# Kernel tuning notes

Hardware: AMD Instinct MI355X
Metric: run time of the kernel (lower is better)

Reference implementation:

```python
import jax, jax.numpy as jnp
import numpy as np

N_EMBD = 1024
N_HEAD = 16
HEAD_DIM = N_EMBD // N_HEAD
LN_EPS = 1e-5


def setup_inputs() -> dict:
    key = jax.random.key(0)
    ks = jax.random.split(key, 8)
    B, T, C = 4, 2048, N_EMBD
    s = lambda fan_in: 1.0 / np.sqrt(fan_in)
    return {
        'x': jax.random.normal(ks[0], (B, T, C), dtype=jnp.float32),
        'w_qkv': jax.random.normal(ks[1], (C, 3 * C), dtype=jnp.float32) * s(C),
        'b_qkv': jnp.zeros((3 * C,), dtype=jnp.float32),
        'ln1_g': jnp.ones((C,), dtype=jnp.float32),
        'ln1_b': jnp.zeros((C,), dtype=jnp.float32),
        'w_fc1': jax.random.normal(ks[2], (C, 4 * C), dtype=jnp.float32) * s(C),
        'b_fc1': jnp.zeros((4 * C,), dtype=jnp.float32),
        'w_fc2': jax.random.normal(ks[3], (4 * C, C), dtype=jnp.float32) * s(4 * C),
        'b_fc2': jnp.zeros((C,), dtype=jnp.float32),
        'ln2_g': jnp.ones((C,), dtype=jnp.float32),
        'ln2_b': jnp.zeros((C,), dtype=jnp.float32),
    }


def _layernorm(x, g, b):
    mu = jnp.mean(x, axis=-1, keepdims=True)
    var = jnp.mean(jnp.square(x - mu), axis=-1, keepdims=True)
    return (x - mu) * jax.lax.rsqrt(var + LN_EPS) * g + b


def _attention(x, w_qkv, b_qkv):
    B, T, C = x.shape
    qkv = x @ w_qkv + b_qkv                      # [B,T,3C]
    q, k, v = jnp.split(qkv, 3, axis=-1)
    q = q.reshape(B, T, N_HEAD, HEAD_DIM)
    k = k.reshape(B, T, N_HEAD, HEAD_DIM)
    v = v.reshape(B, T, N_HEAD, HEAD_DIM)
    scores = jnp.einsum('bqhd,bkhd->bhqk', q, k) / np.sqrt(HEAD_DIM).astype(np.float32)
    causal = jnp.tril(jnp.ones((T, T), dtype=bool))
    scores = jnp.where(causal, scores, -jnp.inf)
    attn = jax.nn.softmax(scores, axis=-1)       # [B,H,T,T]
    y = jnp.einsum('bhqk,bkhd->bqhd', attn, v)
    return y.reshape(B, T, C)


def reference(x, w_qkv, b_qkv, ln1_g, ln1_b, w_fc1, b_fc1, w_fc2, b_fc2, ln2_g, ln2_b):
    # Block: x = ln1(x + attn(x)); x = ln2(x + mlp(x))   (post-LN residual)
    x = _layernorm(x + _attention(x, w_qkv, b_qkv), ln1_g, ln1_b)
    h = jax.nn.gelu(x @ w_fc1 + b_fc1, approximate=False)
    mlp = h @ w_fc2 + b_fc2
    x = _layernorm(x + mlp, ln2_g, ln2_b)
    return x
```

## Files before the change

kernel.cpp:

```cpp
#include <hip/hip_runtime.h>
#include <cstdint>
#include <cstddef>

#define TB 4
#define TT 2048
#define TC 1024
#define NH 16
#define HD 64
#define MROWS (TB * TT)

typedef __bf16 bf16;
typedef unsigned short u16;
typedef __bf16 bf16x8 __attribute__((ext_vector_type(8)));
typedef float floatx4 __attribute__((ext_vector_type(4)));
typedef unsigned short ushort8 __attribute__((ext_vector_type(8)));
typedef unsigned short ushort4v __attribute__((ext_vector_type(4)));

#define LOG2E 1.4426950408889634f

static __device__ __forceinline__ u16 f2bfbits(float f) {
    bf16 b = (bf16)f;
    return __builtin_bit_cast(u16, b);
}

#if __has_builtin(__builtin_amdgcn_exp2f)
#define EXP2F(x) __builtin_amdgcn_exp2f(x)
#else
#define EXP2F(x) exp2f(x)
#endif

static __device__ __forceinline__ void gld_lds16(const u16* g, const u16* lds) {
    __builtin_amdgcn_global_load_lds(
        (const __attribute__((address_space(1))) unsigned int*)(uintptr_t)g,
        (__attribute__((address_space(3))) unsigned int*)(unsigned int)(uintptr_t)lds,
        16, 0, 0);
}

__global__ __launch_bounds__(256) void prep_kernel(
    const float* __restrict__ x, u16* __restrict__ xb,
    const float* __restrict__ w_qkv, u16* __restrict__ wqkvT,
    const float* __restrict__ w_fc1, u16* __restrict__ wfc1T,
    const float* __restrict__ w_fc2, u16* __restrict__ wfc2T)
{
    const int tid = threadIdx.x;
    int blk = blockIdx.x;
    if (blk < 8192) {
        const int i = blk * 256 + tid;
        float4 v = reinterpret_cast<const float4*>(x)[i];
        ushort4v o;
        o.x = f2bfbits(v.x); o.y = f2bfbits(v.y); o.z = f2bfbits(v.z); o.w = f2bfbits(v.w);
        reinterpret_cast<ushort4v*>(xb)[i] = o;
        return;
    }
    blk -= 8192;
    const float* in; u16* out; int K, N, bx, by;
    if (blk < 3072)      { in = w_qkv; out = wqkvT; K = TC;     N = 3 * TC; bx = blk % 96;  by = blk / 96; }
    else if (blk < 7168) { blk -= 3072; in = w_fc1; out = wfc1T; K = TC;    N = 4 * TC; bx = blk & 127; by = blk >> 7; }
    else                 { blk -= 7168; in = w_fc2; out = wfc2T; K = 4 * TC; N = TC;    bx = blk & 31;  by = blk >> 5; }
    __shared__ float tile[32][33];
    const int n0 = bx * 32, k0 = by * 32;
    const int tx = tid & 31, ty = tid >> 5;
    for (int r = 0; r < 32; r += 8)
        tile[ty + r][tx] = in[(size_t)(k0 + ty + r) * N + n0 + tx];
    __syncthreads();
    for (int r = 0; r < 32; r += 8)
        out[(size_t)(n0 + ty + r) * K + k0 + tx] = f2bfbits(tile[tx][ty + r]);
}

template <int GELU>
__global__ __launch_bounds__(512, 2) void gemm256_kernel(
    const u16* __restrict__ A, const u16* __restrict__ Bt,
    const float* __restrict__ bias, u16* __restrict__ Cmat,
    int Nb, int Mt, int Ksz)
{
    __shared__ u16 As[4 * 8192];
    __shared__ u16 Bs[4 * 8192];
    const int tid  = threadIdx.x;
    const int wave = tid >> 6, lane = tid & 63;
    const int quad = lane >> 4, l16 = lane & 15;
    const int wm = (wave >> 2) * 128, wn = (wave & 3) * 64;
    const int Nsz = Nb * 256;
    const int bid = blockIdx.x;
    const int xcd = bid & 7, qb = bid >> 3;
    const int m0 = (xcd * (Mt >> 3) + qb / Nb) * 256;
    const int n0 = (qb % Nb) * 256;

    const int srow = tid >> 2;
    const int sc8  = ((tid & 3) ^ ((tid >> 3) & 3)) * 8;
    const u16* aP = A  + (size_t)(m0 + srow) * Ksz + sc8;
    const u16* bP = Bt + (size_t)(n0 + srow) * Ksz + sc8;
    const size_t half2 = (size_t)128 * Ksz;
    const int sdst = wave * 512;

    const int slot = quad ^ ((l16 >> 1) & 3);
    const int aRd = (wm + l16) * 32 + slot * 8;
    const int bRd = (wn + l16) * 32 + slot * 8;

    floatx4 acc[8][4];
#pragma unroll
    for (int i = 0; i < 8; i++)
#pragma unroll
        for (int j = 0; j < 4; j++)
            acc[i][j] = (floatx4){0.f, 0.f, 0.f, 0.f};

    const int nt = Ksz >> 6;

#define SA(g, kh) do { const u16* s_ = aP + (g) * 64 + (kh) * 32; \
    u16* d_ = As + (((g) & 1) * 2 + (kh)) * 8192 + sdst; \
    gld_lds16(s_, d_); gld_lds16(s_ + half2, d_ + 4096); } while (0)
#define SB(g, kh) do { const u16* s_ = bP + (g) * 64 + (kh) * 32; \
    u16* d_ = Bs + (((g) & 1) * 2 + (kh)) * 8192 + sdst; \
    gld_lds16(s_, d_); gld_lds16(s_ + half2, d_ + 4096); } while (0)

    SA(0, 0); SB(0, 0); SA(0, 1); SB(0, 1); SA(1, 0); SB(1, 0);
    asm volatile("s_waitcnt vmcnt(4)" ::: "memory");
    __builtin_amdgcn_sched_barrier(0);
    __builtin_amdgcn_s_barrier();

#define PHASE(CH, KH, STAGE_STMT, TAILWAIT) do { \
    const u16* ab_ = As + (p * 2 + (KH)) * 8192 + aRd + (CH) * 2048; \
    const u16* bb_ = Bs + (p * 2 + (KH)) * 8192 + bRd; \
    bf16x8 af_[4], bf_[4]; \
    _Pragma("unroll") \
    for (int i_ = 0; i_ < 4; i_++) \
        af_[i_] = *reinterpret_cast<const bf16x8*>(ab_ + i_ * 512); \
    _Pragma("unroll") \
    for (int j_ = 0; j_ < 4; j_++) \
        bf_[j_] = *reinterpret_cast<const bf16x8*>(bb_ + j_ * 512); \
    STAGE_STMT; \
    __builtin_amdgcn_s_barrier(); \
    asm volatile("s_waitcnt lgkmcnt(0)" ::: "memory"); \
    __builtin_amdgcn_sched_barrier(0); \
    __builtin_amdgcn_s_setprio(1); \
    _Pragma("unroll") \
    for (int i_ = 0; i_ < 4; i_++) \
    _Pragma("unroll") \
    for (int j_ = 0; j_ < 4; j_++) \
        acc[(CH) * 4 + i_][j_] = __builtin_amdgcn_mfma_f32_16x16x32_bf16( \
            af_[i_], bf_[j_], acc[(CH) * 4 + i_][j_], 0, 0, 0); \
    __builtin_amdgcn_s_setprio(0); \
    TAILWAIT; \
    __builtin_amdgcn_s_barrier(); \
} while (0)

    for (int g = 0; g < nt; ++g) {
        const int p = g & 1;
        PHASE(0, 0, if (g + 1 < nt) SA(g + 1, 1), );
        PHASE(1, 0, if (g + 1 < nt) SB(g + 1, 1), );
        PHASE(1, 1, if (g + 2 < nt) SA(g + 2, 0), );
        PHASE(0, 1, if (g + 2 < nt) SB(g + 2, 0),
              if (g < nt - 2) { asm volatile("s_waitcnt vmcnt(4)" ::: "memory"); }
              else           { asm volatile("s_waitcnt vmcnt(0)" ::: "memory"); }
              __builtin_amdgcn_sched_barrier(0));
    }
#undef PHASE
#undef SA
#undef SB

    float bv[4];
#pragma unroll
    for (int j = 0; j < 4; j++) bv[j] = bias[n0 + wn + j * 16 + l16];
    const int odd = l16 & 1;
#pragma unroll
    for (int i = 0; i < 8; i++) {
        const int row0 = m0 + wm + i * 16 + quad * 4;
#pragma unroll
        for (int j = 0; j < 4; j++) {
            float v[4];
#pragma unroll
            for (int r = 0; r < 4; r++) {
                float t = acc[i][j][r] + bv[j];
                if (GELU) {
                    float u = t * (0.7978845608f + 0.0356774081f * t * t);
                    float e = EXP2F(u * (2.0f * LOG2E));
                    t = t - t * __builtin_amdgcn_rcpf(e + 1.0f);
                }
                v[r] = t;
            }
            float pv0 = __shfl_xor(v[0], 1), pv1 = __shfl_xor(v[1], 1);
            float pv2 = __shfl_xor(v[2], 1), pv3 = __shfl_xor(v[3], 1);
            float lo0 = odd ? pv2 : v[0];
            float hi0 = odd ? v[2] : pv0;
            float lo1 = odd ? pv3 : v[1];
            float hi1 = odd ? v[3] : pv1;
            unsigned int d0 = (unsigned int)f2bfbits(lo0) | ((unsigned int)f2bfbits(hi0) << 16);
            unsigned int d1 = (unsigned int)f2bfbits(lo1) | ((unsigned int)f2bfbits(hi1) << 16);
            const int row  = row0 + odd * 2;
            const int colp = n0 + wn + j * 16 + (l16 & ~1);
            *reinterpret_cast<unsigned int*>(Cmat + (size_t)row * Nsz + colp)       = d0;
            *reinterpret_cast<unsigned int*>(Cmat + (size_t)(row + 1) * Nsz + colp) = d1;
        }
    }
}

template <int GELU>
__global__ __launch_bounds__(256, 2) void gemm_bt128_kernel(
    const u16* __restrict__ A, const u16* __restrict__ Bt,
    const float* __restrict__ bias, u16* __restrict__ Cmat,
    int Nb, int Ksz)
{
    __shared__ u16 As[128 * 64];
    __shared__ u16 Bs[128 * 64];
    const int tid  = threadIdx.x;
    const int wave = tid >> 6, lane = tid & 63;
    const int quad = lane >> 4, l16 = lane & 15;
    const int Nsz = Nb * 128;
    const int bid = blockIdx.x;
    const int xcd = bid & 7, qb = bid >> 3;
    const int m0 = (xcd * 8 + qb / Nb) * 128;
    const int n0 = (qb % Nb) * 128;
    const int wm = (wave >> 1) * 64, wn = (wave & 1) * 64;

    const int srow = lane >> 3;
    const int scol = ((lane & 7) ^ srow) * 8;
    const u16* ap = A  + (size_t)(m0 + wave * 32 + srow) * Ksz + scol;
    const u16* bp = Bt + (size_t)(n0 + wave * 32 + srow) * Ksz + scol;
    const size_t astep = (size_t)8 * Ksz;

    floatx4 acc[4][4];
#pragma unroll
    for (int i = 0; i < 4; i++)
#pragma unroll
        for (int j = 0; j < 4; j++)
            acc[i][j] = (floatx4){0.f, 0.f, 0.f, 0.f};

    const int l7 = l16 & 7;

    for (int k0 = 0; k0 < Ksz; k0 += 64) {
        __syncthreads();
#pragma unroll
        for (int d = 0; d < 4; d++)
            gld_lds16(ap + d * astep, As + (wave * 4 + d) * 512);
#pragma unroll
        for (int d = 0; d < 4; d++)
            gld_lds16(bp + d * astep, Bs + (wave * 4 + d) * 512);
        ap += 64; bp += 64;
        __syncthreads();

#pragma unroll
        for (int t = 0; t < 2; t++) {
            const int po = ((t * 4 + quad) ^ l7) * 8;
            bf16x8 af[4], bfr[4];
#pragma unroll
            for (int i = 0; i < 4; i++)
                af[i] = *reinterpret_cast<const bf16x8*>(As + (wm + i * 16 + l16) * 64 + po);
#pragma unroll
            for (int j = 0; j < 4; j++)
                bfr[j] = *reinterpret_cast<const bf16x8*>(Bs + (wn + j * 16 + l16) * 64 + po);
#pragma unroll
            for (int i = 0; i < 4; i++)
#pragma unroll
                for (int j = 0; j < 4; j++)
                    acc[i][j] = __builtin_amdgcn_mfma_f32_16x16x32_bf16(af[i], bfr[j], acc[i][j], 0, 0, 0);
        }
    }

    float bv[4];
#pragma unroll
    for (int j = 0; j < 4; j++) bv[j] = bias[n0 + wn + j * 16 + l16];
    const int odd = l16 & 1;
#pragma unroll
    for (int i = 0; i < 4; i++) {
        const int row0 = m0 + wm + i * 16 + quad * 4;
#pragma unroll
        for (int j = 0; j < 4; j++) {
            float v[4];
#pragma unroll
            for (int r = 0; r < 4; r++) {
                float t = acc[i][j][r] + bv[j];
                if (GELU) {
                    float u = t * (0.7978845608f + 0.0356774081f * t * t);
                    float e = EXP2F(u * (2.0f * LOG2E));
                    t = t - t * __builtin_amdgcn_rcpf(e + 1.0f);
                }
                v[r] = t;
            }
            float pv0 = __shfl_xor(v[0], 1), pv1 = __shfl_xor(v[1], 1);
            float pv2 = __shfl_xor(v[2], 1), pv3 = __shfl_xor(v[3], 1);
            float lo0 = odd ? pv2 : v[0];
            float hi0 = odd ? v[2] : pv0;
            float lo1 = odd ? pv3 : v[1];
            float hi1 = odd ? v[3] : pv1;
            unsigned int d0 = (unsigned int)f2bfbits(lo0) | ((unsigned int)f2bfbits(hi0) << 16);
            unsigned int d1 = (unsigned int)f2bfbits(lo1) | ((unsigned int)f2bfbits(hi1) << 16);
            const int row  = row0 + odd * 2;
            const int colp = n0 + wn + j * 16 + (l16 & ~1);
            *reinterpret_cast<unsigned int*>(Cmat + (size_t)row * Nsz + colp)       = d0;
            *reinterpret_cast<unsigned int*>(Cmat + (size_t)(row + 1) * Nsz + colp) = d1;
        }
    }
}

__global__ __launch_bounds__(512) void attn_kernel(const u16* __restrict__ qkv,
                                                   u16* __restrict__ y)
{
    __shared__ u16 Ks[2 * 64 * 64];
    __shared__ u16 Vt[2 * 64 * 64];
    __shared__ u16 Pw[8][16 * 64];
    const int tid  = threadIdx.x;
    const int wave = tid >> 6, lane = tid & 63;
    const int quad = lane >> 4, l16 = lane & 15;
    const int l7   = l16 & 7;
    const int h = blockIdx.y, b = blockIdx.z;
    const int rowbase = b * TT;
    const int S3C = 3 * TC;

    const int srow = (tid >> 3) & 31;
    const int c8   = (tid & 7) * 8;
    const int pcK  = ((tid & 7) ^ (srow & 7)) * 8;
    const int pvb  = (srow + ((tid & 7) << 2)) & 31;
    const bool kRole = (tid < 256);
    const int pcr = (quad ^ l7) * 8;
    unsigned int* const vtw = (unsigned int*)Vt;

    for (int pass = 0; pass < 2; pass++) {
        const int qt   = pass ? (15 - (int)blockIdx.x) : (int)blockIdx.x;
        const int q0b  = qt * 128;
        const int q0w  = q0b + wave * 16;
        const int kend = q0b + 128;

        __syncthreads();

        bf16x8 qf0, qf1;
        {
            const u16* qrow = qkv + (size_t)(rowbase + q0w + l16) * S3C + h * HD + quad * 8;
            bf16x8 t0 = *reinterpret_cast<const bf16x8*>(qrow);
            bf16x8 t1 = *reinterpret_cast<const bf16x8*>(qrow + 32);
#pragma unroll
            for (int i = 0; i < 8; i++) {
                t0[i] = (bf16)((float)t0[i] * (0.125f * LOG2E));
                t1[i] = (bf16)((float)t1[i] * (0.125f * LOG2E));
            }
            qf0 = t0; qf1 = t1;
        }

        float m_s = -__builtin_inff(), l_s = 0.f;
        floatx4 o_acc[4];
#pragma unroll
        for (int n = 0; n < 4; n++) o_acc[n] = (floatx4){0.f, 0.f, 0.f, 0.f};

        const u16* gp = kRole
            ? qkv + (size_t)(rowbase + srow) * S3C + TC + h * HD + c8
            : qkv + (size_t)(rowbase + 2 * srow) * S3C + 2 * TC + h * HD + c8;
        const size_t g2 = kRole ? (size_t)32 * S3C : (size_t)S3C;
        ushort8 r0 = *reinterpret_cast<const ushort8*>(gp);
        ushort8 r1 = *reinterpret_cast<const ushort8*>(gp + g2);

        int buf = 0;
        for (int k0 = 0; k0 < kend; k0 += 64) {
            if (kRole) {
                u16* kb = Ks + buf * 4096;
                *reinterpret_cast<ushort8*>(kb + srow * 64 + pcK)        = r0;
                *reinterpret_cast<ushort8*>(kb + (srow + 32) * 64 + pcK) = r1;
            } else {
                unsigned int* vb = vtw + buf * 2048;
#pragma unroll
                for (int j = 0; j < 8; j++) {
                    unsigned int pk = (unsigned int)r0[j] | ((unsigned int)r1[j] << 16);
                    vb[(c8 + j) * 32 + (pvb ^ (j << 2))] = pk;
                }
            }
            __syncthreads();

            if (k0 + 64 < kend) {
                const u16* gn = gp + (size_t)(k0 + 64) * S3C;
                r0 = *reinterpret_cast<const ushort8*>(gn);
                r1 = *reinterpret_cast<const ushort8*>(gn + g2);
            }

            if (k0 <= q0w + 15) {
                const u16* ksb = Ks + buf * 4096;
                floatx4 st[4];
#pragma unroll
                for (int t = 0; t < 4; t++) {
                    const u16* krowp = ksb + (t * 16 + l16) * 64;
                    bf16x8 ka  = *reinterpret_cast<const bf16x8*>(krowp + pcr);
                    bf16x8 kb2 = *reinterpret_cast<const bf16x8*>(krowp + (pcr ^ 32));
                    floatx4 s = (floatx4){0.f, 0.f, 0.f, 0.f};
                    s = __builtin_amdgcn_mfma_f32_16x16x32_bf16(ka, qf0, s, 0, 0, 0);
                    s = __builtin_amdgcn_mfma_f32_16x16x32_bf16(kb2, qf1, s, 0, 0, 0);
                    st[t] = s;
                }
                float v[16];
                if (k0 + 63 > q0w) {
                    const int kq = k0 - q0w;
#pragma unroll
                    for (int t = 0; t < 4; t++)
#pragma unroll
                        for (int r = 0; r < 4; r++)
                            v[t * 4 + r] = (t * 16 + quad * 4 + r + kq > l16)
                                               ? -__builtin_inff() : st[t][r];
                } else {
#pragma unroll
                    for (int t = 0; t < 4; t++)
#pragma unroll
                        for (int r = 0; r < 4; r++)
                            v[t * 4 + r] = st[t][r];
                }
                float mx = v[0];
#pragma unroll
                for (int i = 1; i < 16; i++) mx = fmaxf(mx, v[i]);
                mx = fmaxf(mx, __shfl_xor(mx, 16));
                mx = fmaxf(mx, __shfl_xor(mx, 32));
                const float mnew  = fmaxf(m_s, mx);
                const float alpha = EXP2F(m_s - mnew);
                float rs = 0.f;
                u16* const pwb = Pw[wave] + l16 * 64;
#pragma unroll
                for (int t = 0; t < 4; t++) {
                    float p0 = EXP2F(v[t * 4 + 0] - mnew);
                    float p1 = EXP2F(v[t * 4 + 1] - mnew);
                    float p2 = EXP2F(v[t * 4 + 2] - mnew);
                    float p3 = EXP2F(v[t * 4 + 3] - mnew);
                    rs += (p0 + p1) + (p2 + p3);
                    ushort4v pk;
                    pk.x = f2bfbits(p0); pk.y = f2bfbits(p1);
                    pk.z = f2bfbits(p2); pk.w = f2bfbits(p3);
                    *reinterpret_cast<ushort4v*>(
                        pwb + ((2 * t + (quad >> 1)) ^ l7) * 8 + (quad & 1) * 4) = pk;
                }
                rs += __shfl_xor(rs, 16);
                rs += __shfl_xor(rs, 32);
                l_s = l_s * alpha + rs;
                m_s = mnew;
#pragma unroll
                for (int n = 0; n < 4; n++) o_acc[n] *= alpha;

                bf16x8 pf0 = *reinterpret_cast<const bf16x8*>(pwb + pcr);
                bf16x8 pf1 = *reinterpret_cast<const bf16x8*>(pwb + (pcr ^ 32));
                const unsigned int* vbb = vtw + buf * 2048;
#pragma unroll
                for (int n = 0; n < 4; n++) {
                    const int dr  = n * 16 + l16;
                    const int pd0 = ((4 * (quad + 2 * n + (l16 >> 3))) & 31) ^ (l7 << 2);
                    bf16x8 vf0 = *reinterpret_cast<const bf16x8*>(vbb + dr * 32 + pd0);
                    bf16x8 vf1 = *reinterpret_cast<const bf16x8*>(vbb + dr * 32 + (pd0 ^ 16));
                    o_acc[n] = __builtin_amdgcn_mfma_f32_16x16x32_bf16(vf0, pf0, o_acc[n], 0, 0, 0);
                    o_acc[n] = __builtin_amdgcn_mfma_f32_16x16x32_bf16(vf1, pf1, o_acc[n], 0, 0, 0);
                }
            }
            buf ^= 1;
        }

        const float li = 1.0f / l_s;
        u16* yrow = y + (size_t)(rowbase + q0w + l16) * TC + h * HD;
#pragma unroll
        for (int n = 0; n < 4; n++) {
            ushort4v ov;
            ov.x = f2bfbits(o_acc[n][0] * li);
            ov.y = f2bfbits(o_acc[n][1] * li);
            ov.z = f2bfbits(o_acc[n][2] * li);
            ov.w = f2bfbits(o_acc[n][3] * li);
            *reinterpret_cast<ushort4v*>(yrow + n * 16 + quad * 4) = ov;
        }
    }
}

template <typename AT, typename OT>
__global__ __launch_bounds__(256) void ln_kernel(
    const AT* __restrict__ a, const bf16* __restrict__ bres,
    const float* __restrict__ g, const float* __restrict__ be,
    OT* __restrict__ out)
{
    const int row = blockIdx.x;
    const int tid = threadIdx.x;
    const size_t base = (size_t)row * TC;
    float v[4];
    for (int i = 0; i < 4; i++) {
        const int c = tid + i * 256;
        v[i] = (float)a[base + c] + (float)bres[base + c];
    }
    float s  = v[0] + v[1] + v[2] + v[3];
    float sq = v[0]*v[0] + v[1]*v[1] + v[2]*v[2] + v[3]*v[3];
    for (int off = 32; off >= 1; off >>= 1) {
        s  += __shfl_xor(s, off, 64);
        sq += __shfl_xor(sq, off, 64);
    }
    __shared__ float red[8];
    const int wv = tid >> 6, lane = tid & 63;
    if (lane == 0) { red[wv] = s; red[4 + wv] = sq; }
    __syncthreads();
    s  = red[0] + red[1] + red[2] + red[3];
    sq = red[4] + red[5] + red[6] + red[7];
    const float mu   = s * (1.0f / TC);
    const float var  = sq * (1.0f / TC) - mu * mu;
    const float rsig = rsqrtf(var + 1e-5f);
    for (int i = 0; i < 4; i++) {
        const int c = tid + i * 256;
        out[base + c] = (OT)((v[i] - mu) * rsig * g[c] + be[c]);
    }
}

extern "C" void kernel_launch(void* const* d_in, const int* in_sizes, int n_in,
                              void* d_out, int out_size, void* d_ws, size_t ws_size,
                              hipStream_t stream)
{
    const float* x     = (const float*)d_in[0];
    const float* w_qkv = (const float*)d_in[1];
    const float* b_qkv = (const float*)d_in[2];
    const float* ln1_g = (const float*)d_in[3];
    const float* ln1_b = (const float*)d_in[4];
    const float* w_fc1 = (const float*)d_in[5];
    const float* b_fc1 = (const float*)d_in[6];
    const float* w_fc2 = (const float*)d_in[7];
    const float* b_fc2 = (const float*)d_in[8];
    const float* ln2_g = (const float*)d_in[9];
    const float* ln2_b = (const float*)d_in[10];
    float* out = (float*)d_out;

    char* ws = (char*)d_ws;
    const size_t MB = 1ull << 20;
    u16* xb    = (u16*)(ws + 0);
    u16* wqkvT = (u16*)(ws + 16 * MB);
    u16* wfc1T = (u16*)(ws + 22 * MB);
    u16* wfc2T = (u16*)(ws + 30 * MB);
    u16* qkv   = (u16*)(ws + 38 * MB);
    u16* yb    = (u16*)(ws + 86 * MB);
    u16* x1    = (u16*)(ws + 102 * MB);
    u16* hb    = (u16*)(ws + 118 * MB);
    u16* mlp   = (u16*)(ws + 38 * MB);

    prep_kernel<<<19456, 256, 0, stream>>>(x, xb, w_qkv, wqkvT, w_fc1, wfc1T, w_fc2, wfc2T);

    gemm256_kernel<0><<<384, 512, 0, stream>>>(xb, wqkvT, b_qkv, qkv, 12, 32, TC);
    attn_kernel<<<dim3(8, NH, TB), 512, 0, stream>>>(qkv, yb);
    ln_kernel<float, bf16><<<MROWS, 256, 0, stream>>>(x, (const bf16*)yb, ln1_g, ln1_b, (bf16*)x1);
    gemm256_kernel<1><<<512, 512, 0, stream>>>((const u16*)x1, wfc1T, b_fc1, hb, 16, 32, TC);
    gemm_bt128_kernel<0><<<8 * 64, 256, 0, stream>>>(hb, wfc2T, b_fc2, mlp, 8, 4 * TC);
    ln_kernel<bf16, float><<<MROWS, 256, 0, stream>>>(
        (const bf16*)x1, (const bf16*)mlp, ln2_g, ln2_b, out);
}
```

Before: 439.0 us.

## Restructure GEMM main loop to cut barriers and reuse B fragments

The bf16 MFMA GEMM main loop used four phases per K-tile, each with two workgroup barriers and a full LDS wait. It now loads LDS fragments for the next MFMA group while the current one runs, and reuses each B fragment set for both A halves instead of reloading it. This leaves two barriers per iteration. The goal is less synchronisation stall and fewer LDS reads, at the cost of more live registers and tighter reasoning about when it is safe to overwrite LDS buffers.

Result: no change. 435.6 us (-0.8%).

```diff
diff --git a/kernel.cpp b/kernel.cpp
--- a/kernel.cpp
+++ b/kernel.cpp
@@ -112,50 +112,66 @@
     u16* d_ = Bs + (((g) & 1) * 2 + (kh)) * 8192 + sdst; \
     gld_lds16(s_, d_); gld_lds16(s_ + half2, d_ + 4096); } while (0)
 
-    SA(0, 0); SB(0, 0); SA(0, 1); SB(0, 1); SA(1, 0); SB(1, 0);
-    asm volatile("s_waitcnt vmcnt(4)" ::: "memory");
-    __builtin_amdgcn_sched_barrier(0);
-    __builtin_amdgcn_s_barrier();
-
-#define PHASE(CH, KH, STAGE_STMT, TAILWAIT) do { \
-    const u16* ab_ = As + (p * 2 + (KH)) * 8192 + aRd + (CH) * 2048; \
-    const u16* bb_ = Bs + (p * 2 + (KH)) * 8192 + bRd; \
-    bf16x8 af_[4], bf_[4]; \
+#define LDA(dst, CH, KH) do { \
+    const u16* b_ = As + (p * 2 + (KH)) * 8192 + aRd + (CH) * 2048; \
     _Pragma("unroll") \
     for (int i_ = 0; i_ < 4; i_++) \
-        af_[i_] = *reinterpret_cast<const bf16x8*>(ab_ + i_ * 512); \
+        dst[i_] = *reinterpret_cast<const bf16x8*>(b_ + i_ * 512); } while (0)
+#define LDB(dst, KH) do { \
+    const u16* b_ = Bs + (p * 2 + (KH)) * 8192 + bRd; \
     _Pragma("unroll") \
     for (int j_ = 0; j_ < 4; j_++) \
-        bf_[j_] = *reinterpret_cast<const bf16x8*>(bb_ + j_ * 512); \
-    STAGE_STMT; \
-    __builtin_amdgcn_s_barrier(); \
-    asm volatile("s_waitcnt lgkmcnt(0)" ::: "memory"); \
-    __builtin_amdgcn_sched_barrier(0); \
+        dst[j_] = *reinterpret_cast<const bf16x8*>(b_ + j_ * 512); } while (0)
+#define MM(CH, AF, BF) do { \
     __builtin_amdgcn_s_setprio(1); \
     _Pragma("unroll") \
     for (int i_ = 0; i_ < 4; i_++) \
     _Pragma("unroll") \
     for (int j_ = 0; j_ < 4; j_++) \
         acc[(CH) * 4 + i_][j_] = __builtin_amdgcn_mfma_f32_16x16x32_bf16( \
-            af_[i_], bf_[j_], acc[(CH) * 4 + i_][j_], 0, 0, 0); \
-    __builtin_amdgcn_s_setprio(0); \
-    TAILWAIT; \
-    __builtin_amdgcn_s_barrier(); \
-} while (0)
+            AF[i_], BF[j_], acc[(CH) * 4 + i_][j_], 0, 0, 0); \
+    __builtin_amdgcn_s_setprio(0); } while (0)
+
+    SA(0, 0); SB(0, 0); SA(0, 1); SB(0, 1); SA(1, 0); SB(1, 0);
+    asm volatile("s_waitcnt vmcnt(4)" ::: "memory");
+    __builtin_amdgcn_sched_barrier(0);
+    __builtin_amdgcn_s_barrier();
+    __builtin_amdgcn_sched_barrier(0);
 
     for (int g = 0; g < nt; ++g) {
         const int p = g & 1;
-        PHASE(0, 0, if (g + 1 < nt) SA(g + 1, 1), );
-        PHASE(1, 0, if (g + 1 < nt) SB(g + 1, 1), );
-        PHASE(1, 1, if (g + 2 < nt) SA(g + 2, 0), );
-        PHASE(0, 1, if (g + 2 < nt) SB(g + 2, 0),
-              if (g < nt - 2) { asm volatile("s_waitcnt vmcnt(4)" ::: "memory"); }
-              else           { asm volatile("s_waitcnt vmcnt(0)" ::: "memory"); }
-              __builtin_amdgcn_sched_barrier(0));
-    }
-#undef PHASE
+        bf16x8 aF[4], aG[4], b0[4], b1[4];
+        LDA(aF, 0, 0); LDB(b0, 0);
+        LDA(aG, 1, 0);
+        if (g + 1 < nt) SA(g + 1, 1);
+        __builtin_amdgcn_sched_barrier(0);
+        MM(0, aF, b0);
+        LDA(aF, 1, 1); LDB(b1, 1);
+        if (g + 1 < nt) SB(g + 1, 1);
+        __builtin_amdgcn_sched_barrier(0);
+        MM(1, aG, b0);
+        __builtin_amdgcn_s_barrier();
+        __builtin_amdgcn_sched_barrier(0);
+        LDA(aG, 0, 1);
+        if (g + 2 < nt) SA(g + 2, 0);
+        __builtin_amdgcn_sched_barrier(0);
+        MM(1, aF, b1);
+        if (g + 2 < nt) SB(g + 2, 0);
+        __builtin_amdgcn_sched_barrier(0);
+        MM(0, aG, b1);
+        if (g + 1 < nt) {
+            if (g < nt - 2) { asm volatile("s_waitcnt vmcnt(4)" ::: "memory"); }
+            else            { asm volatile("s_waitcnt vmcnt(0)" ::: "memory"); }
+            __builtin_amdgcn_sched_barrier(0);
+            __builtin_amdgcn_s_barrier();
+            __builtin_amdgcn_sched_barrier(0);
+        }
+    }
+#undef MM
+#undef LDB
+#undef LDA
+#undef SB
 #undef SA
-#undef SB
 
     float bv[4];
 #pragma unroll
```
